# Optimization experiments

Hardware: AMD Instinct MI355X
Metric: run time of the kernel (lower is better)

## Reference

```python
import jax, jax.numpy as jnp
import numpy as np

N_NODES = 65536   # N
D_HID   = 128     # D (hidden)
N_GROUPS = 16384  # G portfolios
GROUP_LEN = 64    # lines per portfolio (port_len entries)
N_LINES = N_GROUPS * GROUP_LEN  # L
BATCH = 16384     # B samples


def setup_inputs() -> dict:
    key = jax.random.key(0)
    k = jax.random.split(key, 5)
    H = jax.random.normal(k[0], (N_NODES, D_HID), dtype=jnp.float32)
    port_w_signed_flat = jax.random.normal(k[1], (N_LINES,), dtype=jnp.float32)
    anchor_idx = jax.random.randint(k[2], (BATCH,), 0, N_NODES, dtype=jnp.int32)
    pf_gid = jax.random.randint(k[3], (BATCH,), 0, N_GROUPS, dtype=jnp.int32)
    port_nodes_flat = jax.random.randint(k[4], (N_LINES,), 0, N_NODES, dtype=jnp.int32)
    port_len = jnp.full((N_GROUPS,), GROUP_LEN, dtype=jnp.int32)
    return {
        'H': H,
        'port_w_signed_flat': port_w_signed_flat,
        'anchor_idx': anchor_idx,
        'pf_gid': pf_gid,
        'port_nodes_flat': port_nodes_flat,
        'port_len': port_len,
    }


def reference(H, port_w_signed_flat, anchor_idx, pf_gid, port_nodes_flat, port_len):
    """Faithful, vectorized port of compute_samplewise_portfolio_vectors_loo.

    Ragged segment-weighted mean per portfolio group, with strict leave-one-out
    correction for each sample's anchor node, followed by L2 normalization.
    Returns (V_abs, V_sgn), each [B, D].
    """
    N, D = H.shape
    G = port_len.shape[0]
    L = port_nodes_flat.shape[0]

    # gid per flat line: repeat_interleave(arange(G), lens)
    gid_lines = jnp.repeat(jnp.arange(G, dtype=jnp.int32), port_len,
                           total_repeat_length=L)

    w_abs = jnp.abs(port_w_signed_flat)
    Hl = H[port_nodes_flat]                                  # [L, D] gather
    S_abs = jax.ops.segment_sum(w_abs[:, None] * Hl, gid_lines, num_segments=G)
    W_abs = jax.ops.segment_sum(w_abs, gid_lines, num_segments=G)
    W_sgn = jax.ops.segment_sum(port_w_signed_flat, gid_lines, num_segments=G)

    valid = (pf_gid >= 0) & (pf_gid < G)
    g = jnp.clip(pf_gid, 0, G - 1)

    # Leave-one-out self-weight: sum of w over lines where (gid==g_i, node==anchor_i).
    # Vectorized join via a sorted composite int32 key (G*N < 2^31 by construction).
    keys_l = gid_lines * N + port_nodes_flat                 # [L]
    keys_s = g * N + anchor_idx                              # [B]
    order = jnp.argsort(keys_l)
    sk = keys_l[order]
    zero1 = jnp.zeros((1,), H.dtype)
    ca = jnp.concatenate([zero1, jnp.cumsum(w_abs[order])])
    cs = jnp.concatenate([zero1, jnp.cumsum(port_w_signed_flat[order])])
    lo = jnp.searchsorted(sk, keys_s, side='left')
    hi = jnp.searchsorted(sk, keys_s, side='right')
    self_w_abs = ca[hi] - ca[lo]                             # [B]
    self_w_sgn = cs[hi] - cs[lo]                             # [B]

    Ha = H[anchor_idx]                                       # [B, D]
    denom = jnp.maximum(W_abs[g] - self_w_abs, 1e-12)        # clamp_min
    V_abs = (S_abs[g] - self_w_abs[:, None] * Ha) / denom[:, None]
    V_sgn = ((W_sgn[g] - self_w_sgn) / denom)[:, None] * V_abs

    V_abs = jnp.where(valid[:, None], V_abs, jnp.zeros((), H.dtype))
    V_sgn = jnp.where(valid[:, None], V_sgn, jnp.zeros((), H.dtype))

    # torch F.normalize: x / clamp(||x||, min=eps)
    na = jnp.linalg.norm(V_abs, axis=1, keepdims=True)
    V_abs = V_abs / jnp.maximum(na, 1e-6)
    ns = jnp.linalg.norm(V_sgn, axis=1, keepdims=True)
    V_sgn = jnp.where(ns > 0, V_sgn / jnp.maximum(ns, 1e-6), V_sgn)
    return V_abs, V_sgn
```

## Files before the change

kernel.cpp:

```cpp
#include <hip/hip_runtime.h>
#include <hip/hip_bf16.h>


#define DDIM 128

__device__ inline unsigned bf_rne(float x) {
    unsigned u = __float_as_uint(x);
    return (u + 0x7FFFu + ((u >> 16) & 1u)) >> 16;
}

__device__ inline void unpack2(unsigned d, float& lo, float& hi) {
    lo = __uint_as_float(d << 16);
    hi = __uint_as_float(d & 0xFFFF0000u);
}

__global__ __launch_bounds__(1024) void init_kernel(
    const float4* __restrict__ H4, uint2* __restrict__ Hb, int n4,
    const int* __restrict__ plen, int* __restrict__ offs, int G,
    const int* __restrict__ pf_gid, int* __restrict__ used, int B, int nconv) {
    const int t = threadIdx.x;
    const int bb = blockIdx.x;
    if (bb < nconv) {
        const int i = bb * 1024 + t;
        if (i < n4) {
            const float4 v = H4[i];
            uint2 o;
            o.x = bf_rne(v.x) | (bf_rne(v.y) << 16);
            o.y = bf_rne(v.z) | (bf_rne(v.w) << 16);
            Hb[i] = o;
        }
        return;
    }
    if (bb == nconv) {
        for (int i = t; i < G; i += 1024) used[i] = 0;
        __syncthreads();
        for (int i = t; i < B; i += 1024) {
            const int g = pf_gid[i];
            if (g >= 0 && g < G) used[g] = 1;
        }
        return;
    }
    __shared__ int part[1024];
    const int chunk = (G + 1023) >> 10;
    const int lo = min(t * chunk, G);
    const int hi = min(lo + chunk, G);
    int s = 0;
    for (int i = lo; i < hi; ++i) s += plen[i];
    part[t] = s;
    __syncthreads();
    #pragma unroll
    for (int ofs = 1; ofs < 1024; ofs <<= 1) {
        int v = (t >= ofs) ? part[t - ofs] : 0;
        __syncthreads();
        part[t] += v;
        __syncthreads();
    }
    int run = part[t] - s;
    for (int i = lo; i < hi; ++i) { offs[i] = run; run += plen[i]; }
}

__global__ __launch_bounds__(256) void group_sums(
    const unsigned short* __restrict__ Hb,
    const float* __restrict__ pw, const int* __restrict__ pn,
    const int* __restrict__ plen, const int* __restrict__ offs,
    const int* __restrict__ used,
    float* __restrict__ Sabs, float* __restrict__ Wag,
    float* __restrict__ Wsg, int G) {
    const int g = blockIdx.x * 4 + (threadIdx.x >> 6);
    if (g >= G) return;
    if (!used[g]) return;
    const int lane = threadIdx.x & 63;
    const int q = lane >> 4;
    const int s = lane & 15;

    const int off = offs[g];
    const int len = plen[g];

    float acc[8] = {0.f, 0.f, 0.f, 0.f, 0.f, 0.f, 0.f, 0.f};
    float laWa = 0.f, laWs = 0.f;

    for (int base = 0; base < len; base += 64) {
        float wl = 0.f;
        int nl = 0;
        if (base + lane < len) {
            wl = pw[off + base + lane];
            nl = pn[off + base + lane];
        }
        laWa += fabsf(wl);
        laWs += wl;

        #pragma unroll
        for (int jj = 0; jj < 64; jj += 4) {
            const float ww = fabsf(__shfl(wl, jj + q));
            const int row = __shfl(nl, jj + q);
            const uint4 h = *((const uint4*)(Hb + (size_t)row * DDIM) + s);
            float f0, f1, f2, f3, f4, f5, f6, f7;
            unpack2(h.x, f0, f1);
            unpack2(h.y, f2, f3);
            unpack2(h.z, f4, f5);
            unpack2(h.w, f6, f7);
            acc[0] = fmaf(ww, f0, acc[0]);
            acc[1] = fmaf(ww, f1, acc[1]);
            acc[2] = fmaf(ww, f2, acc[2]);
            acc[3] = fmaf(ww, f3, acc[3]);
            acc[4] = fmaf(ww, f4, acc[4]);
            acc[5] = fmaf(ww, f5, acc[5]);
            acc[6] = fmaf(ww, f6, acc[6]);
            acc[7] = fmaf(ww, f7, acc[7]);
        }
    }

    #pragma unroll
    for (int m = 32; m; m >>= 1) {
        laWa += __shfl_xor(laWa, m);
        laWs += __shfl_xor(laWs, m);
    }
    #pragma unroll
    for (int k = 0; k < 8; ++k) {
        acc[k] += __shfl_xor(acc[k], 16);
        acc[k] += __shfl_xor(acc[k], 32);
    }

    if (q == 0) {
        float4* dst = (float4*)(Sabs + (size_t)g * DDIM + 8 * s);
        dst[0] = make_float4(acc[0], acc[1], acc[2], acc[3]);
        dst[1] = make_float4(acc[4], acc[5], acc[6], acc[7]);
    }
    if (lane == 0) { Wag[g] = laWa; Wsg[g] = laWs; }
}

__global__ __launch_bounds__(256) void per_sample(
    const unsigned short* __restrict__ Hb,
    const float* __restrict__ pw, const int* __restrict__ pn,
    const int* __restrict__ plen, const int* __restrict__ offs,
    const float* __restrict__ Sabs, const float* __restrict__ Wag,
    const float* __restrict__ Wsg,
    const int* __restrict__ anchor_idx, const int* __restrict__ pf_gid,
    float* __restrict__ out, int B, int G) {
    const int b = blockIdx.x * (blockDim.x >> 6) + (threadIdx.x >> 6);
    const int lane = threadIdx.x & 63;
    if (b >= B) return;

    float2* outA = (float2*)(out + (size_t)b * DDIM);
    float2* outS = (float2*)(out + ((size_t)B + b) * DDIM);

    const int g = pf_gid[b];
    if (!(g >= 0 && g < G)) {
        const float2 z = make_float2(0.f, 0.f);
        outA[lane] = z;
        outS[lane] = z;
        return;
    }

    const int anchor = anchor_idx[b];
    const int off = offs[g];
    const int len = plen[g];

    float selfa = 0.f, selfs = 0.f;
    for (int base = 0; base < len; base += 64) {
        const int jmax = min(64, len - base);
        if (lane < jmax) {
            const float w = pw[off + base + lane];
            const int n = pn[off + base + lane];
            if (n == anchor) { selfa += fabsf(w); selfs += w; }
        }
    }
    #pragma unroll
    for (int m = 32; m; m >>= 1) {
        selfa += __shfl_xor(selfa, m);
        selfs += __shfl_xor(selfs, m);
    }

    const float Wa = Wag[g];
    const float Wsn = Wsg[g];
    const float2 S = ((const float2*)(Sabs + (size_t)g * DDIM))[lane];
    const unsigned hb = *((const unsigned*)(Hb + (size_t)anchor * DDIM) + lane);
    float h0, h1;
    unpack2(hb, h0, h1);

    const float denom = fmaxf(Wa - selfa, 1e-12f);
    float2 v;
    v.x = (S.x - selfa * h0) / denom;
    v.y = (S.y - selfa * h1) / denom;
    const float scale = (Wsn - selfs) / denom;

    float n2 = v.x * v.x + v.y * v.y;
    #pragma unroll
    for (int m = 32; m; m >>= 1) n2 += __shfl_xor(n2, m);
    const float na = sqrtf(n2);

    const float invA = 1.0f / fmaxf(na, 1e-6f);
    const float ns = fabsf(scale) * na;
    const float sgnscale = (ns > 0.f) ? (scale / fmaxf(ns, 1e-6f)) : scale;

    outA[lane] = make_float2(v.x * invA, v.y * invA);
    outS[lane] = make_float2(v.x * sgnscale, v.y * sgnscale);
}

__global__ __launch_bounds__(1024) void scan_only(
    const int* __restrict__ len, int* __restrict__ offs, int G) {
    __shared__ int part[1024];
    const int t = threadIdx.x;
    const int chunk = (G + 1023) >> 10;
    const int lo = min(t * chunk, G);
    const int hi = min(lo + chunk, G);
    int s = 0;
    for (int i = lo; i < hi; ++i) s += len[i];
    part[t] = s;
    __syncthreads();
    #pragma unroll
    for (int ofs = 1; ofs < 1024; ofs <<= 1) {
        int v = (t >= ofs) ? part[t - ofs] : 0;
        __syncthreads();
        part[t] += v;
        __syncthreads();
    }
    int run = part[t] - s;
    for (int i = lo; i < hi; ++i) { offs[i] = run; run += len[i]; }
}

__global__ __launch_bounds__(256) void pf_loo_f32(
    const float* __restrict__ H, const float* __restrict__ pw,
    const int* __restrict__ anchor_idx, const int* __restrict__ pf_gid,
    const int* __restrict__ pn, const int* __restrict__ plen,
    const int* __restrict__ offs, float* __restrict__ out, int B, int G) {
    const int b = blockIdx.x * (blockDim.x >> 6) + (threadIdx.x >> 6);
    const int lane = threadIdx.x & 63;
    const int half = lane >> 5;
    const int qlane = lane & 31;
    if (b >= B) return;
    float4* outA = (float4*)(out + (size_t)b * DDIM);
    float4* outS = (float4*)(out + ((size_t)B + b) * DDIM);
    const int gid = pf_gid[b];
    if (!(gid >= 0 && gid < G)) {
        float4 z = make_float4(0.f, 0.f, 0.f, 0.f);
        if (half == 0) { outA[qlane] = z; outS[qlane] = z; }
        return;
    }
    const int anchor = anchor_idx[b];
    const int off = offs[gid];
    const int len = plen[gid];
    float4 acc = make_float4(0.f, 0.f, 0.f, 0.f);
    float laWa = 0.f, laWs = 0.f, laSa = 0.f, laSs = 0.f;
    for (int base = 0; base < len; base += 64) {
        const int jmax = min(64, len - base);
        float wl = 0.f;
        int nl = -1;
        if (lane < jmax) { wl = pw[off + base + lane]; nl = pn[off + base + lane]; }
        const float wla = fabsf(wl);
        laWa += wla; laWs += wl;
        if (nl == anchor) { laSa += wla; laSs += wl; }
        #pragma unroll 8
        for (int jj = 0; jj < 64; jj += 2) {
            const float ww = fabsf(__shfl(wl, jj + half));
            const int row = __shfl(nl, jj + half);
            const float4 h = ((const float4*)(H + (size_t)row * DDIM))[qlane];
            acc.x = fmaf(ww, h.x, acc.x);
            acc.y = fmaf(ww, h.y, acc.y);
            acc.z = fmaf(ww, h.z, acc.z);
            acc.w = fmaf(ww, h.w, acc.w);
        }
    }
    #pragma unroll
    for (int m = 32; m; m >>= 1) {
        laWa += __shfl_xor(laWa, m);
        laWs += __shfl_xor(laWs, m);
        laSa += __shfl_xor(laSa, m);
        laSs += __shfl_xor(laSs, m);
    }
    acc.x += __shfl_xor(acc.x, 32);
    acc.y += __shfl_xor(acc.y, 32);
    acc.z += __shfl_xor(acc.z, 32);
    acc.w += __shfl_xor(acc.w, 32);
    const float denom = fmaxf(laWa - laSa, 1e-12f);
    const float4 hv = ((const float4*)(H + (size_t)anchor * DDIM))[qlane];
    float4 v;
    v.x = (acc.x - laSa * hv.x) / denom;
    v.y = (acc.y - laSa * hv.y) / denom;
    v.z = (acc.z - laSa * hv.z) / denom;
    v.w = (acc.w - laSa * hv.w) / denom;
    const float scale = (laWs - laSs) / denom;
    float n2 = v.x * v.x + v.y * v.y + v.z * v.z + v.w * v.w;
    #pragma unroll
    for (int m = 32; m; m >>= 1) n2 += __shfl_xor(n2, m);
    n2 *= 0.5f;
    const float na = sqrtf(n2);
    const float invA = 1.0f / fmaxf(na, 1e-6f);
    const float ns = fabsf(scale) * na;
    const float sgnscale = (ns > 0.f) ? (scale / fmaxf(ns, 1e-6f)) : scale;
    const float sc = half ? sgnscale : invA;
    float4 res = make_float4(v.x * sc, v.y * sc, v.z * sc, v.w * sc);
    float4* dst = half ? outS : outA;
    dst[qlane] = res;
}

extern "C" void kernel_launch(void* const* d_in, const int* in_sizes, int n_in,
                              void* d_out, int out_size, void* d_ws, size_t ws_size,
                              hipStream_t stream) {
    const float* H      = (const float*)d_in[0];
    const float* pw     = (const float*)d_in[1];
    const int* anchor   = (const int*)d_in[2];
    const int* gid      = (const int*)d_in[3];
    const int* pn       = (const int*)d_in[4];
    const int* plen     = (const int*)d_in[5];
    float* out          = (float*)d_out;

    const int B = in_sizes[2];
    const int G = in_sizes[5];
    const int ND = in_sizes[0];
    const size_t hb_bytes = (size_t)ND * 2;
    const size_t sabs_bytes = (size_t)G * DDIM * 4;
    const size_t need = hb_bytes + sabs_bytes + (size_t)G * 4 * 4;

    if (ws_size >= need) {
        char* p = (char*)d_ws;
        unsigned short* Hb = (unsigned short*)p;        p += hb_bytes;
        float* Sabs        = (float*)p;                 p += sabs_bytes;
        int* offsp         = (int*)p;                   p += (size_t)G * 4;
        int* usedp         = (int*)p;                   p += (size_t)G * 4;
        float* Wag         = (float*)p;                 p += (size_t)G * 4;
        float* Wsg         = (float*)p;

        const int n4 = ND / 4;
        const int nconv = (n4 + 1023) / 1024;
        init_kernel<<<nconv + 2, 1024, 0, stream>>>(
            (const float4*)H, (uint2*)Hb, n4, plen, offsp, G, gid, usedp, B, nconv);

        const int gblocks = (G + 3) / 4;
        group_sums<<<gblocks, 256, 0, stream>>>(Hb, pw, pn, plen, offsp, usedp,
                                                Sabs, Wag, Wsg, G);

        const int sblocks = (B + 3) / 4;
        per_sample<<<sblocks, 256, 0, stream>>>(Hb, pw, pn, plen, offsp, Sabs,
                                                Wag, Wsg, anchor, gid, out, B, G);
    } else {
        int* offsp = (int*)d_ws;
        scan_only<<<1, 1024, 0, stream>>>(plen, offsp, G);
        const int blocks = (B + 3) / 4;
        pf_loo_f32<<<blocks, 256, 0, stream>>>(H, pw, anchor, gid, pn, plen,
                                               offsp, out, B, G);
    }
}
```

Measured before the change: 141.7 us.

## Split bf16 H into column planes so each XCD gathers from one plane

The bf16 copy of H is rewritten into 8 column planes of 16 features each. `group_sums` launches 8 blocks per group set, with the plane chosen as blockIdx&7. With round-robin block dispatch across XCDs, each XCD should then gather only from a roughly 2MB plane that can stay resident in its L2, instead of making random row gathers over the full 16MB table. The trade-offs are smaller 8-byte-per-lane gather segments and reading each group's weight and index lists 8 times. Separately, `per_sample` now reads the anchor row from fp32 H rather than the bf16 copy.

```diff
diff --git a/kernel.cpp b/kernel.cpp
--- a/kernel.cpp
+++ b/kernel.cpp
@@ -15,7 +15,7 @@
 }
 
 __global__ __launch_bounds__(1024) void init_kernel(
-    const float4* __restrict__ H4, uint2* __restrict__ Hb, int n4,
+    const float4* __restrict__ H4, uint2* __restrict__ Hb, int n4, int N,
     const int* __restrict__ plen, int* __restrict__ offs, int G,
     const int* __restrict__ pf_gid, int* __restrict__ used, int B, int nconv) {
     const int t = threadIdx.x;
@@ -27,7 +27,10 @@
             uint2 o;
             o.x = bf_rne(v.x) | (bf_rne(v.y) << 16);
             o.y = bf_rne(v.z) | (bf_rne(v.w) << 16);
-            Hb[i] = o;
+            const int n = i >> 5;
+            const int j = i & 31;
+            const int cc = j >> 2;
+            Hb[(size_t)cc * ((size_t)N * 4) + n * 4 + (j & 3)] = o;
         }
         return;
     }
@@ -60,23 +63,26 @@
 }
 
 __global__ __launch_bounds__(256) void group_sums(
-    const unsigned short* __restrict__ Hb,
+    const unsigned short* __restrict__ Hp,
     const float* __restrict__ pw, const int* __restrict__ pn,
     const int* __restrict__ plen, const int* __restrict__ offs,
     const int* __restrict__ used,
     float* __restrict__ Sabs, float* __restrict__ Wag,
-    float* __restrict__ Wsg, int G) {
-    const int g = blockIdx.x * 4 + (threadIdx.x >> 6);
+    float* __restrict__ Wsg, int G, int N) {
+    const int b = blockIdx.x;
+    const int c = b & 7;
+    const int g = (b >> 3) * 4 + (threadIdx.x >> 6);
     if (g >= G) return;
     if (!used[g]) return;
     const int lane = threadIdx.x & 63;
-    const int q = lane >> 4;
-    const int s = lane & 15;
+    const int q = lane >> 2;
+    const int s = lane & 3;
+    const unsigned short* plane = Hp + (size_t)c * ((size_t)N * 16);
 
     const int off = offs[g];
     const int len = plen[g];
 
-    float acc[8] = {0.f, 0.f, 0.f, 0.f, 0.f, 0.f, 0.f, 0.f};
+    float acc0 = 0.f, acc1 = 0.f, acc2 = 0.f, acc3 = 0.f;
     float laWa = 0.f, laWs = 0.f;
 
     for (int base = 0; base < len; base += 64) {
@@ -86,51 +92,47 @@
             wl = pw[off + base + lane];
             nl = pn[off + base + lane];
         }
-        laWa += fabsf(wl);
-        laWs += wl;
+        if (c == 0) { laWa += fabsf(wl); laWs += wl; }
 
         #pragma unroll
-        for (int jj = 0; jj < 64; jj += 4) {
-            const float ww = fabsf(__shfl(wl, jj + q));
-            const int row = __shfl(nl, jj + q);
-            const uint4 h = *((const uint4*)(Hb + (size_t)row * DDIM) + s);
-            float f0, f1, f2, f3, f4, f5, f6, f7;
+        for (int it = 0; it < 4; ++it) {
+            const int src = it * 16 + q;
+            const float ww = fabsf(__shfl(wl, src));
+            const int row = __shfl(nl, src);
+            const uint2 h = *(const uint2*)(plane + (size_t)row * 16 + s * 4);
+            float f0, f1, f2, f3;
             unpack2(h.x, f0, f1);
             unpack2(h.y, f2, f3);
-            unpack2(h.z, f4, f5);
-            unpack2(h.w, f6, f7);
-            acc[0] = fmaf(ww, f0, acc[0]);
-            acc[1] = fmaf(ww, f1, acc[1]);
-            acc[2] = fmaf(ww, f2, acc[2]);
-            acc[3] = fmaf(ww, f3, acc[3]);
-            acc[4] = fmaf(ww, f4, acc[4]);
-            acc[5] = fmaf(ww, f5, acc[5]);
-            acc[6] = fmaf(ww, f6, acc[6]);
-            acc[7] = fmaf(ww, f7, acc[7]);
-        }
-    }
-
-    #pragma unroll
-    for (int m = 32; m; m >>= 1) {
-        laWa += __shfl_xor(laWa, m);
-        laWs += __shfl_xor(laWs, m);
-    }
-    #pragma unroll
-    for (int k = 0; k < 8; ++k) {
-        acc[k] += __shfl_xor(acc[k], 16);
-        acc[k] += __shfl_xor(acc[k], 32);
-    }
-
-    if (q == 0) {
-        float4* dst = (float4*)(Sabs + (size_t)g * DDIM + 8 * s);
-        dst[0] = make_float4(acc[0], acc[1], acc[2], acc[3]);
-        dst[1] = make_float4(acc[4], acc[5], acc[6], acc[7]);
-    }
-    if (lane == 0) { Wag[g] = laWa; Wsg[g] = laWs; }
+            acc0 = fmaf(ww, f0, acc0);
+            acc1 = fmaf(ww, f1, acc1);
+            acc2 = fmaf(ww, f2, acc2);
+            acc3 = fmaf(ww, f3, acc3);
+        }
+    }
+
+    #pragma unroll
+    for (int m = 4; m < 64; m <<= 1) {
+        acc0 += __shfl_xor(acc0, m);
+        acc1 += __shfl_xor(acc1, m);
+        acc2 += __shfl_xor(acc2, m);
+        acc3 += __shfl_xor(acc3, m);
+    }
+    if (lane < 4) {
+        float4* dst = (float4*)(Sabs + (size_t)g * DDIM + c * 16 + 4 * lane);
+        *dst = make_float4(acc0, acc1, acc2, acc3);
+    }
+    if (c == 0) {
+        #pragma unroll
+        for (int m = 32; m; m >>= 1) {
+            laWa += __shfl_xor(laWa, m);
+            laWs += __shfl_xor(laWs, m);
+        }
+        if (lane == 0) { Wag[g] = laWa; Wsg[g] = laWs; }
+    }
 }
 
 __global__ __launch_bounds__(256) void per_sample(
-    const unsigned short* __restrict__ Hb,
+    const float* __restrict__ H,
     const float* __restrict__ pw, const int* __restrict__ pn,
     const int* __restrict__ plen, const int* __restrict__ offs,
     const float* __restrict__ Sabs, const float* __restrict__ Wag,
@@ -174,14 +176,12 @@
     const float Wa = Wag[g];
     const float Wsn = Wsg[g];
     const float2 S = ((const float2*)(Sabs + (size_t)g * DDIM))[lane];
-    const unsigned hb = *((const unsigned*)(Hb + (size_t)anchor * DDIM) + lane);
-    float h0, h1;
-    unpack2(hb, h0, h1);
+    const float2 hv = ((const float2*)(H + (size_t)anchor * DDIM))[lane];
 
     const float denom = fmaxf(Wa - selfa, 1e-12f);
     float2 v;
-    v.x = (S.x - selfa * h0) / denom;
-    v.y = (S.y - selfa * h1) / denom;
+    v.x = (S.x - selfa * hv.x) / denom;
+    v.y = (S.y - selfa * hv.y) / denom;
     const float scale = (Wsn - selfs) / denom;
 
     float n2 = v.x * v.x + v.y * v.y;
@@ -308,6 +308,7 @@
     const int B = in_sizes[2];
     const int G = in_sizes[5];
     const int ND = in_sizes[0];
+    const int N  = ND / DDIM;
     const size_t hb_bytes = (size_t)ND * 2;
     const size_t sabs_bytes = (size_t)G * DDIM * 4;
     const size_t need = hb_bytes + sabs_bytes + (size_t)G * 4 * 4;
@@ -324,14 +325,14 @@
         const int n4 = ND / 4;
         const int nconv = (n4 + 1023) / 1024;
         init_kernel<<<nconv + 2, 1024, 0, stream>>>(
-            (const float4*)H, (uint2*)Hb, n4, plen, offsp, G, gid, usedp, B, nconv);
-
-        const int gblocks = (G + 3) / 4;
+            (const float4*)H, (uint2*)Hb, n4, N, plen, offsp, G, gid, usedp, B, nconv);
+
+        const int gblocks = ((G + 3) / 4) * 8;
         group_sums<<<gblocks, 256, 0, stream>>>(Hb, pw, pn, plen, offsp, usedp,
-                                                Sabs, Wag, Wsg, G);
+                                                Sabs, Wag, Wsg, G, N);
 
         const int sblocks = (B + 3) / 4;
-        per_sample<<<sblocks, 256, 0, stream>>>(Hb, pw, pn, plen, offsp, Sabs,
+        per_sample<<<sblocks, 256, 0, stream>>>(H, pw, pn, plen, offsp, Sabs,
                                                 Wag, Wsg, anchor, gid, out, B, G);
     } else {
         int* offsp = (int*)d_ws;
```

New measurement: 159.7 us. 1.13x slower.

## Move leave-one-out self-weight scan into group-sum launch to overlap work

Applied to the files above, without the earlier changes.

Takes the per-sample scan for the anchor's self-weight out of the final per-sample kernel and runs it as extra blocks of the group-sum launch, writing the results to new workspace buffers. The per-sample epilogue then only reads those precomputed values. The aim is to let the latency-bound line scans run alongside the gather-heavy group sums and to make the epilogue lighter. The cost is an extra round trip through global memory for the self-weights and a larger workspace requirement.

```diff
diff --git a/kernel.cpp b/kernel.cpp
--- a/kernel.cpp
+++ b/kernel.cpp
@@ -59,82 +59,115 @@
     for (int i = lo; i < hi; ++i) { offs[i] = run; run += plen[i]; }
 }
 
-__global__ __launch_bounds__(256) void group_sums(
+__global__ __launch_bounds__(256) void mid_kernel(
     const unsigned short* __restrict__ Hb,
     const float* __restrict__ pw, const int* __restrict__ pn,
     const int* __restrict__ plen, const int* __restrict__ offs,
     const int* __restrict__ used,
     float* __restrict__ Sabs, float* __restrict__ Wag,
-    float* __restrict__ Wsg, int G) {
-    const int g = blockIdx.x * 4 + (threadIdx.x >> 6);
-    if (g >= G) return;
-    if (!used[g]) return;
+    float* __restrict__ Wsg,
+    const int* __restrict__ anchor_idx, const int* __restrict__ pf_gid,
+    float* __restrict__ selfa_buf, float* __restrict__ selfs_buf,
+    int G, int B, int gb) {
     const int lane = threadIdx.x & 63;
-    const int q = lane >> 4;
-    const int s = lane & 15;
-
+    const int wid = threadIdx.x >> 6;
+
+    if (blockIdx.x < gb) {
+        const int g = blockIdx.x * 4 + wid;
+        if (g >= G) return;
+        if (!used[g]) return;
+        const int q = lane >> 4;
+        const int s = lane & 15;
+
+        const int off = offs[g];
+        const int len = plen[g];
+
+        float acc[8] = {0.f, 0.f, 0.f, 0.f, 0.f, 0.f, 0.f, 0.f};
+        float laWa = 0.f, laWs = 0.f;
+
+        for (int base = 0; base < len; base += 64) {
+            float wl = 0.f;
+            int nl = 0;
+            if (base + lane < len) {
+                wl = pw[off + base + lane];
+                nl = pn[off + base + lane];
+            }
+            laWa += fabsf(wl);
+            laWs += wl;
+
+            #pragma unroll
+            for (int jj = 0; jj < 64; jj += 4) {
+                const float ww = fabsf(__shfl(wl, jj + q));
+                const int row = __shfl(nl, jj + q);
+                const uint4 h = *((const uint4*)(Hb + (size_t)row * DDIM) + s);
+                float f0, f1, f2, f3, f4, f5, f6, f7;
+                unpack2(h.x, f0, f1);
+                unpack2(h.y, f2, f3);
+                unpack2(h.z, f4, f5);
+                unpack2(h.w, f6, f7);
+                acc[0] = fmaf(ww, f0, acc[0]);
+                acc[1] = fmaf(ww, f1, acc[1]);
+                acc[2] = fmaf(ww, f2, acc[2]);
+                acc[3] = fmaf(ww, f3, acc[3]);
+                acc[4] = fmaf(ww, f4, acc[4]);
+                acc[5] = fmaf(ww, f5, acc[5]);
+                acc[6] = fmaf(ww, f6, acc[6]);
+                acc[7] = fmaf(ww, f7, acc[7]);
+            }
+        }
+
+        #pragma unroll
+        for (int m = 32; m; m >>= 1) {
+            laWa += __shfl_xor(laWa, m);
+            laWs += __shfl_xor(laWs, m);
+        }
+        #pragma unroll
+        for (int k = 0; k < 8; ++k) {
+            acc[k] += __shfl_xor(acc[k], 16);
+            acc[k] += __shfl_xor(acc[k], 32);
+        }
+
+        if (q == 0) {
+            float4* dst = (float4*)(Sabs + (size_t)g * DDIM + 8 * s);
+            dst[0] = make_float4(acc[0], acc[1], acc[2], acc[3]);
+            dst[1] = make_float4(acc[4], acc[5], acc[6], acc[7]);
+        }
+        if (lane == 0) { Wag[g] = laWa; Wsg[g] = laWs; }
+        return;
+    }
+
+    const int b = (blockIdx.x - gb) * 4 + wid;
+    if (b >= B) return;
+    const int g = pf_gid[b];
+    if (!(g >= 0 && g < G)) {
+        if (lane == 0) { selfa_buf[b] = 0.f; selfs_buf[b] = 0.f; }
+        return;
+    }
+    const int anchor = anchor_idx[b];
     const int off = offs[g];
     const int len = plen[g];
 
-    float acc[8] = {0.f, 0.f, 0.f, 0.f, 0.f, 0.f, 0.f, 0.f};
-    float laWa = 0.f, laWs = 0.f;
-
+    float selfa = 0.f, selfs = 0.f;
     for (int base = 0; base < len; base += 64) {
-        float wl = 0.f;
-        int nl = 0;
         if (base + lane < len) {
-            wl = pw[off + base + lane];
-            nl = pn[off + base + lane];
-        }
-        laWa += fabsf(wl);
-        laWs += wl;
-
-        #pragma unroll
-        for (int jj = 0; jj < 64; jj += 4) {
-            const float ww = fabsf(__shfl(wl, jj + q));
-            const int row = __shfl(nl, jj + q);
-            const uint4 h = *((const uint4*)(Hb + (size_t)row * DDIM) + s);
-            float f0, f1, f2, f3, f4, f5, f6, f7;
-            unpack2(h.x, f0, f1);
-            unpack2(h.y, f2, f3);
-            unpack2(h.z, f4, f5);
-            unpack2(h.w, f6, f7);
-            acc[0] = fmaf(ww, f0, acc[0]);
-            acc[1] = fmaf(ww, f1, acc[1]);
-            acc[2] = fmaf(ww, f2, acc[2]);
-            acc[3] = fmaf(ww, f3, acc[3]);
-            acc[4] = fmaf(ww, f4, acc[4]);
-            acc[5] = fmaf(ww, f5, acc[5]);
-            acc[6] = fmaf(ww, f6, acc[6]);
-            acc[7] = fmaf(ww, f7, acc[7]);
-        }
-    }
-
+            const float w = pw[off + base + lane];
+            const int n = pn[off + base + lane];
+            if (n == anchor) { selfa += fabsf(w); selfs += w; }
+        }
+    }
     #pragma unroll
     for (int m = 32; m; m >>= 1) {
-        laWa += __shfl_xor(laWa, m);
-        laWs += __shfl_xor(laWs, m);
-    }
-    #pragma unroll
-    for (int k = 0; k < 8; ++k) {
-        acc[k] += __shfl_xor(acc[k], 16);
-        acc[k] += __shfl_xor(acc[k], 32);
-    }
-
-    if (q == 0) {
-        float4* dst = (float4*)(Sabs + (size_t)g * DDIM + 8 * s);
-        dst[0] = make_float4(acc[0], acc[1], acc[2], acc[3]);
-        dst[1] = make_float4(acc[4], acc[5], acc[6], acc[7]);
-    }
-    if (lane == 0) { Wag[g] = laWa; Wsg[g] = laWs; }
-}
-
-__global__ __launch_bounds__(256) void per_sample(
+        selfa += __shfl_xor(selfa, m);
+        selfs += __shfl_xor(selfs, m);
+    }
+    if (lane == 0) { selfa_buf[b] = selfa; selfs_buf[b] = selfs; }
+}
+
+__global__ __launch_bounds__(256) void epi_kernel(
     const unsigned short* __restrict__ Hb,
-    const float* __restrict__ pw, const int* __restrict__ pn,
-    const int* __restrict__ plen, const int* __restrict__ offs,
     const float* __restrict__ Sabs, const float* __restrict__ Wag,
     const float* __restrict__ Wsg,
+    const float* __restrict__ selfa_buf, const float* __restrict__ selfs_buf,
     const int* __restrict__ anchor_idx, const int* __restrict__ pf_gid,
     float* __restrict__ out, int B, int G) {
     const int b = blockIdx.x * (blockDim.x >> 6) + (threadIdx.x >> 6);
@@ -153,24 +186,8 @@
     }
 
     const int anchor = anchor_idx[b];
-    const int off = offs[g];
-    const int len = plen[g];
-
-    float selfa = 0.f, selfs = 0.f;
-    for (int base = 0; base < len; base += 64) {
-        const int jmax = min(64, len - base);
-        if (lane < jmax) {
-            const float w = pw[off + base + lane];
-            const int n = pn[off + base + lane];
-            if (n == anchor) { selfa += fabsf(w); selfs += w; }
-        }
-    }
-    #pragma unroll
-    for (int m = 32; m; m >>= 1) {
-        selfa += __shfl_xor(selfa, m);
-        selfs += __shfl_xor(selfs, m);
-    }
-
+    const float selfa = selfa_buf[b];
+    const float selfs = selfs_buf[b];
     const float Wa = Wag[g];
     const float Wsn = Wsg[g];
     const float2 S = ((const float2*)(Sabs + (size_t)g * DDIM))[lane];
@@ -310,7 +327,8 @@
     const int ND = in_sizes[0];
     const size_t hb_bytes = (size_t)ND * 2;
     const size_t sabs_bytes = (size_t)G * DDIM * 4;
-    const size_t need = hb_bytes + sabs_bytes + (size_t)G * 4 * 4;
+    const size_t need = hb_bytes + sabs_bytes + (size_t)G * 4 * 4
+                        + (size_t)B * 4 * 2;
 
     if (ws_size >= need) {
         char* p = (char*)d_ws;
@@ -319,20 +337,25 @@
         int* offsp         = (int*)p;                   p += (size_t)G * 4;
         int* usedp         = (int*)p;                   p += (size_t)G * 4;
         float* Wag         = (float*)p;                 p += (size_t)G * 4;
-        float* Wsg         = (float*)p;
+        float* Wsg         = (float*)p;                 p += (size_t)G * 4;
+        float* selfa_buf   = (float*)p;                 p += (size_t)B * 4;
+        float* selfs_buf   = (float*)p;
 
         const int n4 = ND / 4;
         const int nconv = (n4 + 1023) / 1024;
         init_kernel<<<nconv + 2, 1024, 0, stream>>>(
             (const float4*)H, (uint2*)Hb, n4, plen, offsp, G, gid, usedp, B, nconv);
 
-        const int gblocks = (G + 3) / 4;
-        group_sums<<<gblocks, 256, 0, stream>>>(Hb, pw, pn, plen, offsp, usedp,
-                                                Sabs, Wag, Wsg, G);
-
-        const int sblocks = (B + 3) / 4;
-        per_sample<<<sblocks, 256, 0, stream>>>(Hb, pw, pn, plen, offsp, Sabs,
-                                                Wag, Wsg, anchor, gid, out, B, G);
+        const int gb = (G + 3) / 4;
+        const int sb = (B + 3) / 4;
+        mid_kernel<<<gb + sb, 256, 0, stream>>>(Hb, pw, pn, plen, offsp, usedp,
+                                                Sabs, Wag, Wsg, anchor, gid,
+                                                selfa_buf, selfs_buf, G, B, gb);
+
+        const int eb = (B + 3) / 4;
+        epi_kernel<<<eb, 256, 0, stream>>>(Hb, Sabs, Wag, Wsg,
+                                           selfa_buf, selfs_buf,
+                                           anchor, gid, out, B, G);
     } else {
         int* offsp = (int*)d_ws;
         scan_only<<<1, 1024, 0, stream>>>(plen, offsp, G);
```

New measurement: 146.3 us. 1.03x slower.
